# Performance work log

Hardware: AMD Instinct MI355X
Metric: run time of the kernel (lower is better)

## Reference

```python
import jax, jax.numpy as jnp
import numpy as np

E = 256   # embedding_channels
C = 128   # c
N1 = 512
N2 = 512
NE1 = 16384
NE2 = 16384
EPS = 1e-5


def _ln(x, w, b):
    m = x.mean(-1, keepdims=True)
    v = jnp.mean((x - m) ** 2, axis=-1, keepdims=True)
    return (x - m) * jax.lax.rsqrt(v + EPS) * w + b


def _lin(x, w, b):
    return x @ w.T + b


def setup_inputs() -> dict:
    key = jax.random.key(0)
    ks = jax.random.split(key, 12)
    p = lambda k, shape: jax.random.normal(k, shape, jnp.float32) * 0.02
    return {
        "z": jax.random.normal(ks[0], (N1, N2, E), jnp.float32),
        "efeat1": jax.random.normal(ks[1], (NE1, E), jnp.float32),
        "efeat2": jax.random.normal(ks[2], (NE2, E), jnp.float32),
        "ln_w": jnp.ones((E,), jnp.float32), "ln_b": jnp.zeros((E,), jnp.float32),
        "lnc_w": jnp.ones((C,), jnp.float32), "lnc_b": jnp.zeros((C,), jnp.float32),
        "gl1_w": p(ks[3], (C, E)), "gl1_b": jnp.zeros((C,), jnp.float32),
        "gl2_w": p(ks[4], (C, E)), "gl2_b": jnp.zeros((C,), jnp.float32),
        "l1_w": p(ks[5], (C, E)), "l1_b": jnp.zeros((C,), jnp.float32),
        "l2_w": p(ks[6], (C, E)), "l2_b": jnp.zeros((C,), jnp.float32),
        "eg_w": p(ks[7], (E, E)), "eg_b": jnp.zeros((E,), jnp.float32),
        "las_w": p(ks[8], (E, C)), "las_b": jnp.zeros((E,), jnp.float32),
        "edges1": jax.random.randint(ks[9], (2, NE1), 0, N1, jnp.int64 if jax.config.jax_enable_x64 else jnp.int32),
        "edges2": jax.random.randint(ks[10], (2, NE2), 0, N2, jnp.int64 if jax.config.jax_enable_x64 else jnp.int32),
    }


def reference(z, efeat1, efeat2, ln_w, ln_b, lnc_w, lnc_b, gl1_w, gl1_b,
              gl2_w, gl2_b, l1_w, l1_b, l2_w, l2_b, eg_w, eg_b,
              las_w, las_b, edges1, edges2):
    zl = _ln(z, ln_w, ln_b)                       # [n1,n2,E]
    p1 = _ln(efeat1, ln_w, ln_b)                  # [ne1,E]
    p2 = _ln(efeat2, ln_w, ln_b)                  # [ne2,E]

    gate = lambda x, gw, gb, lw, lb: jax.nn.sigmoid(_lin(x, gw, gb)) * _lin(x, lw, lb)
    ab1 = gate(zl, gl1_w, gl1_b, l1_w, l1_b)      # [n1,n2,C]
    ab2 = gate(zl, gl2_w, gl2_b, l2_w, l2_b)      # [n1,n2,C]
    p1 = gate(p1, gl1_w, gl1_b, l1_w, l1_b)       # [ne1,C]
    p2 = gate(p2, gl2_w, gl2_b, l2_w, l2_b)       # [ne2,C]
    g = jax.nn.sigmoid(_lin(zl, eg_w, eg_b))      # [n1,n2,E]

    n1, n2 = z.shape[0], z.shape[1]
    # sparse COO -> dense (duplicate indices sum, matching torch coalesce)
    P1 = jnp.zeros((n1, n1, C), z.dtype).at[edges1[0], edges1[1]].add(p1)
    P2 = jnp.zeros((n2, n2, C), z.dtype).at[edges2[0], edges2[1]].add(p2)

    block1 = jnp.einsum('ikc,kjc->ijc', P1, ab1)  # [n1,n2,C]
    block2 = jnp.einsum('ikc,jkc->ijc', ab2, P2)  # [n1,n2,C]

    return g * _lin(_ln(block1 + block2, lnc_w, lnc_b), las_w, las_b)
```

## Files before the change

kernel.cpp:

```cpp
#include <hip/hip_runtime.h>
#include <stdint.h>

#define NN 512
#define EE 256
#define CC 128
#define NEDGE 16384
#define RR (NN*NN)
#define RT3 (RR + 2*NEDGE)

using bf16x8 = __attribute__((ext_vector_type(8))) short;
using f32x4  = __attribute__((ext_vector_type(4))) float;

__device__ __forceinline__ unsigned short f2bf(float f) {
  union { float f; unsigned u; } v; v.f = f;
  unsigned r = v.u + 0x7FFFu + ((v.u >> 16) & 1u);
  return (unsigned short)(r >> 16);
}
__device__ __forceinline__ float bf2f(unsigned short h) {
  union { unsigned u; float f; } v; v.u = ((unsigned)h) << 16;
  return v.f;
}
__device__ __forceinline__ float sigm(float x) { return 1.f / (1.f + __expf(-x)); }

__global__ __launch_bounds__(256) void k_ln(
    const float* __restrict__ z, const float* __restrict__ e1,
    const float* __restrict__ e2, const float* __restrict__ lnw,
    const float* __restrict__ lnb, unsigned short* __restrict__ zl) {
  int row = blockIdx.x * 4 + (threadIdx.x >> 6);
  int lane = threadIdx.x & 63;
  const float* src;
  if (row < RR)            src = z  + (size_t)row * EE;
  else if (row < RR+NEDGE) src = e1 + (size_t)(row - RR) * EE;
  else                     src = e2 + (size_t)(row - RR - NEDGE) * EE;
  float4 v = ((const float4*)src)[lane];
  float s = v.x + v.y + v.z + v.w;
  float q = v.x*v.x + v.y*v.y + v.z*v.z + v.w*v.w;
  #pragma unroll
  for (int o = 32; o > 0; o >>= 1) { s += __shfl_xor(s, o); q += __shfl_xor(q, o); }
  float m = s * (1.f/EE);
  float rstd = rsqrtf(q*(1.f/EE) - m*m + 1e-5f);
  float4 wv = ((const float4*)lnw)[lane];
  float4 bv = ((const float4*)lnb)[lane];
  ushort4 o4;
  o4.x = f2bf((v.x - m)*rstd*wv.x + bv.x);
  o4.y = f2bf((v.y - m)*rstd*wv.y + bv.y);
  o4.z = f2bf((v.z - m)*rstd*wv.z + bv.z);
  o4.w = f2bf((v.w - m)*rstd*wv.w + bv.w);
  ((ushort4*)(zl + (size_t)row * EE))[lane] = o4;
}

__global__ __launch_bounds__(256) void k_wconv(
    const float* __restrict__ gl1, const float* __restrict__ l1,
    const float* __restrict__ gl2, const float* __restrict__ l2,
    const float* __restrict__ eg,  const float* __restrict__ las,
    unsigned short* __restrict__ Wcol, unsigned short* __restrict__ Wrow,
    unsigned short* __restrict__ Wlas) {
  int t = blockIdx.x * 256 + threadIdx.x;
  if (t < 65536) {
    Wcol[t] = f2bf(t < 32768 ? gl1[t] : l1[t - 32768]);
  } else if (t < 196608) {
    int u = t - 65536;
    float v = (u < 32768) ? gl2[u] : (u < 65536) ? l2[u - 32768] : eg[u - 65536];
    Wrow[u] = f2bf(v);
  } else {
    int u = t - 196608;
    Wlas[u] = f2bf(las[u]);
  }
}

__global__ __launch_bounds__(256) void k_proj_gate(
    const unsigned short* __restrict__ zl, const unsigned short* __restrict__ W,
    const float* __restrict__ gb, const float* __restrict__ lb,
    unsigned short* __restrict__ abOut, float* __restrict__ Pf,
    const int* __restrict__ edges, int mode) {
  __shared__ __attribute__((aligned(16))) short As[128*32];
  __shared__ __attribute__((aligned(16))) short Bg[128*32];
  __shared__ __attribute__((aligned(16))) short Bl[128*32];
  const int t = threadIdx.x, w = t >> 6, lane = t & 63;
  const int mt = blockIdx.x;
  const bool isE = (mt >= RR/128);
  size_t abase; int astride;
  if (!isE) {
    if (mode == 0) { int rt0 = mt*128; abase = (size_t)(rt0 & 511)*512 + (rt0 >> 9); astride = 512; }
    else           { abase = (size_t)mt*128; astride = 1; }
  } else {
    abase = (size_t)RR + (mode ? NEDGE : 0) + (mt*128 - RR); astride = 1;
  }
  const f32x4 z4 = {0.f, 0.f, 0.f, 0.f};
  f32x4 ag[4][4], al[4][4];
  #pragma unroll
  for (int a = 0; a < 4; ++a)
    #pragma unroll
    for (int b = 0; b < 4; ++b) { ag[a][b] = z4; al[a][b] = z4; }
  const int wr = (w >> 1)*64, wc = (w & 1)*64;
  #pragma unroll 1
  for (int kk = 0; kk < 8; ++kk) {
    const int k0 = kk * 32;
    __syncthreads();
    #pragma unroll
    for (int s2 = 0; s2 < 2; ++s2) {
      int sidx = t + s2*256, row = sidx >> 2, seg = sidx & 3;
      int lo = row*32 + seg*8;
      *(uint4*)&As[lo] = *(const uint4*)(zl + (abase + (size_t)row*astride)*EE + k0 + seg*8);
      const unsigned short* wp = W + (size_t)row*EE + k0 + seg*8;
      *(uint4*)&Bg[lo] = *(const uint4*)wp;
      *(uint4*)&Bl[lo] = *(const uint4*)(wp + 128*EE);
    }
    __syncthreads();
    bf16x8 af[4], bgf[4], blf[4];
    #pragma unroll
    for (int f = 0; f < 4; ++f) {
      af[f]  = *(const bf16x8*)&As[(wr + f*16 + (lane & 15))*32 + (lane >> 4)*8];
      bgf[f] = *(const bf16x8*)&Bg[(wc + f*16 + (lane & 15))*32 + (lane >> 4)*8];
      blf[f] = *(const bf16x8*)&Bl[(wc + f*16 + (lane & 15))*32 + (lane >> 4)*8];
    }
    #pragma unroll
    for (int fm = 0; fm < 4; ++fm)
      #pragma unroll
      for (int fn = 0; fn < 4; ++fn) {
        ag[fm][fn] = __builtin_amdgcn_mfma_f32_16x16x32_bf16(af[fm], bgf[fn], ag[fm][fn], 0, 0, 0);
        al[fm][fn] = __builtin_amdgcn_mfma_f32_16x16x32_bf16(af[fm], blf[fn], al[fm][fn], 0, 0, 0);
      }
  }
  const int quad = lane >> 4, lc = lane & 15;
  #pragma unroll
  for (int fm = 0; fm < 4; ++fm)
    #pragma unroll
    for (int fn = 0; fn < 4; ++fn) {
      int c = wc + fn*16 + lc;
      float bgv = gb[c], blv = lb[c];
      float v0 = sigm(ag[fm][fn][0] + bgv) * (al[fm][fn][0] + blv);
      float v1 = sigm(ag[fm][fn][1] + bgv) * (al[fm][fn][1] + blv);
      float v2 = sigm(ag[fm][fn][2] + bgv) * (al[fm][fn][2] + blv);
      float v3 = sigm(ag[fm][fn][3] + bgv) * (al[fm][fn][3] + blv);
      int rl = wr + fm*16 + quad*4;
      if (!isE) {
        size_t rt = (size_t)mt*128 + rl;
        ushort4 o; o.x = f2bf(v0); o.y = f2bf(v1); o.z = f2bf(v2); o.w = f2bf(v3);
        *(ushort4*)&abOut[(size_t)c*RR + rt] = o;
      } else {
        int e0 = mt*128 - RR + rl;
        float vv[4] = {v0, v1, v2, v3};
        #pragma unroll
        for (int rg = 0; rg < 4; ++rg) {
          int e = e0 + rg;
          int i0 = edges[e], i1 = edges[NEDGE + e];
          atomicAdd(&Pf[((size_t)i0*NN + i1)*CC + c], vv[rg]);
        }
      }
    }
}

__global__ __launch_bounds__(256) void k_proj_g(
    const unsigned short* __restrict__ zl, const unsigned short* __restrict__ Weg,
    const float* __restrict__ egb, unsigned short* __restrict__ gOut) {
  __shared__ __attribute__((aligned(16))) short As[128*32];
  __shared__ __attribute__((aligned(16))) short Bs[128*32];
  const int t = threadIdx.x, w = t >> 6, lane = t & 63;
  const int mt = blockIdx.x, half = blockIdx.y;
  const size_t abase = (size_t)mt * 128;
  const unsigned short* Wb = Weg + (size_t)half * 128 * EE;
  const f32x4 z4 = {0.f, 0.f, 0.f, 0.f};
  f32x4 acc[4][4];
  #pragma unroll
  for (int a = 0; a < 4; ++a)
    #pragma unroll
    for (int b = 0; b < 4; ++b) acc[a][b] = z4;
  const int wr = (w >> 1)*64, wc = (w & 1)*64;
  #pragma unroll 1
  for (int kk = 0; kk < 8; ++kk) {
    const int k0 = kk * 32;
    __syncthreads();
    #pragma unroll
    for (int s2 = 0; s2 < 2; ++s2) {
      int sidx = t + s2*256, row = sidx >> 2, seg = sidx & 3;
      int lo = row*32 + seg*8;
      *(uint4*)&As[lo] = *(const uint4*)(zl + (abase + row)*EE + k0 + seg*8);
      *(uint4*)&Bs[lo] = *(const uint4*)(Wb + (size_t)row*EE + k0 + seg*8);
    }
    __syncthreads();
    bf16x8 af[4], bf_[4];
    #pragma unroll
    for (int f = 0; f < 4; ++f) {
      af[f]  = *(const bf16x8*)&As[(wr + f*16 + (lane & 15))*32 + (lane >> 4)*8];
      bf_[f] = *(const bf16x8*)&Bs[(wc + f*16 + (lane & 15))*32 + (lane >> 4)*8];
    }
    #pragma unroll
    for (int fn = 0; fn < 4; ++fn)
      #pragma unroll
      for (int fm = 0; fm < 4; ++fm)
        acc[fn][fm] = __builtin_amdgcn_mfma_f32_16x16x32_bf16(bf_[fn], af[fm], acc[fn][fm], 0, 0, 0);
  }
  const int quad = lane >> 4, lc = lane & 15;
  #pragma unroll
  for (int fn = 0; fn < 4; ++fn) {
    int e = half*128 + wc + fn*16 + quad*4;
    float4 bv = *(const float4*)(egb + e);
    #pragma unroll
    for (int fm = 0; fm < 4; ++fm) {
      size_t r = (size_t)mt*128 + wr + fm*16 + lc;
      ushort4 o;
      o.x = f2bf(sigm(acc[fn][fm][0] + bv.x));
      o.y = f2bf(sigm(acc[fn][fm][1] + bv.y));
      o.z = f2bf(sigm(acc[fn][fm][2] + bv.z));
      o.w = f2bf(sigm(acc[fn][fm][3] + bv.w));
      *(ushort4*)&gOut[r*EE + e] = o;
    }
  }
}

__global__ __launch_bounds__(256) void k_pcvt(
    const float* __restrict__ P1f, const float* __restrict__ P2f,
    unsigned short* __restrict__ P1c, unsigned short* __restrict__ P2c) {
  const float* src = blockIdx.y ? P2f : P1f;
  unsigned short* dst = blockIdx.y ? P2c : P1c;
  __shared__ float Ls[128*65];
  const int t = threadIdx.x;
  const size_t pos0 = (size_t)blockIdx.x * 64;
  #pragma unroll
  for (int it = 0; it < 8; ++it) {
    int fi = t + it*256;
    int p = fi >> 5, cq = fi & 31;
    float4 v = ((const float4*)(src + (pos0 + p)*CC))[cq];
    Ls[(cq*4+0)*65 + p] = v.x; Ls[(cq*4+1)*65 + p] = v.y;
    Ls[(cq*4+2)*65 + p] = v.z; Ls[(cq*4+3)*65 + p] = v.w;
  }
  __syncthreads();
  #pragma unroll
  for (int it = 0; it < 8; ++it) {
    int oi = t + it*256;
    int c = oi >> 4, pq = oi & 15;
    ushort4 o;
    o.x = f2bf(Ls[c*65 + pq*4 + 0]); o.y = f2bf(Ls[c*65 + pq*4 + 1]);
    o.z = f2bf(Ls[c*65 + pq*4 + 2]); o.w = f2bf(Ls[c*65 + pq*4 + 3]);
    *(ushort4*)&dst[(size_t)c*RR + pos0 + pq*4] = o;
  }
}

__global__ __launch_bounds__(256) void k_einsum(
    const unsigned short* __restrict__ P1c, const unsigned short* __restrict__ ab1t,
    const unsigned short* __restrict__ ab2c, const unsigned short* __restrict__ P2c,
    float* __restrict__ Sf) {
  __shared__ __attribute__((aligned(16))) short A1s[128*32];
  __shared__ __attribute__((aligned(16))) short B1s[128*32];
  __shared__ __attribute__((aligned(16))) short A2s[128*32];
  __shared__ __attribute__((aligned(16))) short B2s[128*32];
  const int t = threadIdx.x, w = t >> 6, lane = t & 63;
  const int n = blockIdx.x;
  const int xcd = n & 7, bi = n >> 3;
  const int ch = xcd * 16 + (bi >> 4);
  const int tile = bi & 15;
  const int mt = tile & 3, nt = tile >> 2;
  const size_t cb = (size_t)ch * RR;
  const unsigned short* A1g = P1c  + cb + (size_t)mt*128*512;
  const unsigned short* B1g = ab1t + cb + (size_t)nt*128*512;
  const unsigned short* A2g = ab2c + cb + (size_t)mt*128*512;
  const unsigned short* B2g = P2c  + cb + (size_t)nt*128*512;
  const f32x4 z4 = {0.f, 0.f, 0.f, 0.f};
  f32x4 acc[4][4];
  #pragma unroll
  for (int a = 0; a < 4; ++a)
    #pragma unroll
    for (int b = 0; b < 4; ++b) acc[a][b] = z4;
  const int wr = (w >> 1)*64, wc = (w & 1)*64;
  #pragma unroll 1
  for (int kk = 0; kk < 16; ++kk) {
    const int k0 = kk * 32;
    __syncthreads();
    #pragma unroll
    for (int s2 = 0; s2 < 2; ++s2) {
      int sidx = t + s2*256, row = sidx >> 2, seg = sidx & 3;
      int go = row*512 + k0 + seg*8;
      int lo = row*32 + seg*8;
      *(uint4*)&A1s[lo] = *(const uint4*)(A1g + go);
      *(uint4*)&B1s[lo] = *(const uint4*)(B1g + go);
      *(uint4*)&A2s[lo] = *(const uint4*)(A2g + go);
      *(uint4*)&B2s[lo] = *(const uint4*)(B2g + go);
    }
    __syncthreads();
    bf16x8 a1[4], b1[4], a2[4], b2[4];
    #pragma unroll
    for (int f = 0; f < 4; ++f) {
      int ro = (wr + f*16 + (lane & 15))*32 + (lane >> 4)*8;
      int co = (wc + f*16 + (lane & 15))*32 + (lane >> 4)*8;
      a1[f] = *(const bf16x8*)&A1s[ro];
      a2[f] = *(const bf16x8*)&A2s[ro];
      b1[f] = *(const bf16x8*)&B1s[co];
      b2[f] = *(const bf16x8*)&B2s[co];
    }
    #pragma unroll
    for (int fm = 0; fm < 4; ++fm)
      #pragma unroll
      for (int fn = 0; fn < 4; ++fn) {
        acc[fm][fn] = __builtin_amdgcn_mfma_f32_16x16x32_bf16(a1[fm], b1[fn], acc[fm][fn], 0, 0, 0);
        acc[fm][fn] = __builtin_amdgcn_mfma_f32_16x16x32_bf16(a2[fm], b2[fn], acc[fm][fn], 0, 0, 0);
      }
  }
  const int quad = lane >> 4, lc = lane & 15;
  #pragma unroll
  for (int fm = 0; fm < 4; ++fm)
    #pragma unroll
    for (int fn = 0; fn < 4; ++fn) {
      int j = nt*128 + wc + fn*16 + lc;
      int ib = mt*128 + wr + fm*16 + quad*4;
      #pragma unroll
      for (int rg = 0; rg < 4; ++rg)
        Sf[cb + (size_t)(ib + rg)*NN + j] = acc[fm][fn][rg];
    }
}

__global__ __launch_bounds__(256) void k_out(
    const float* __restrict__ Sf, const unsigned short* __restrict__ g,
    const unsigned short* __restrict__ Wlas, const float* __restrict__ lasb,
    const float* __restrict__ lncw, const float* __restrict__ lncb,
    float* __restrict__ out) {
  __shared__ __attribute__((aligned(16))) char Als[64*256];
  const int t = threadIdx.x, w = t >> 6, lane = t & 63;
  const size_t r0 = (size_t)blockIdx.x * 64;
  const int row = t >> 2, part = t & 3;

  float x[32];
  const float* sp = Sf + (size_t)(part*32)*RR + r0 + row;
  #pragma unroll
  for (int i = 0; i < 32; ++i) x[i] = sp[(size_t)i*RR];
  float s = 0.f, q = 0.f;
  #pragma unroll
  for (int i = 0; i < 32; ++i) { s += x[i]; q += x[i]*x[i]; }
  s += __shfl_xor(s, 1); q += __shfl_xor(q, 1);
  s += __shfl_xor(s, 2); q += __shfl_xor(q, 2);
  float m = s * (1.f/CC);
  float rstd = rsqrtf(q*(1.f/CC) - m*m + 1e-5f);

  {
    const float4* wv4 = (const float4*)(lncw + part*32);
    const float4* bv4 = (const float4*)(lncb + part*32);
    #pragma unroll
    for (int i4 = 0; i4 < 8; ++i4) {
      float4 wv = wv4[i4], bv = bv4[i4];
      ushort4 o;
      o.x = f2bf((x[i4*4+0]-m)*rstd*wv.x + bv.x);
      o.y = f2bf((x[i4*4+1]-m)*rstd*wv.y + bv.y);
      o.z = f2bf((x[i4*4+2]-m)*rstd*wv.z + bv.z);
      o.w = f2bf((x[i4*4+3]-m)*rstd*wv.w + bv.w);
      int boff = (part*64 + i4*8) ^ ((row & 7) << 4);
      *(ushort4*)(Als + row*256 + boff) = o;
    }
  }
  __syncthreads();

  const int quad = lane >> 4, lc = lane & 15;
  const f32x4 z4 = {0.f, 0.f, 0.f, 0.f};
  f32x4 acc[4][4];
  #pragma unroll
  for (int a = 0; a < 4; ++a)
    #pragma unroll
    for (int b = 0; b < 4; ++b) acc[a][b] = z4;
  #pragma unroll
  for (int kk = 0; kk < 4; ++kk) {
    bf16x8 wf[4], sfr[4];
    #pragma unroll
    for (int f = 0; f < 4; ++f) {
      wf[f]  = *(const bf16x8*)(Wlas + (size_t)(w*64 + f*16 + lc)*CC + kk*32 + quad*8);
      int r = f*16 + lc;
      sfr[f] = *(const bf16x8*)(Als + r*256 + ((kk*64 + quad*16) ^ ((r & 7) << 4)));
    }
    #pragma unroll
    for (int fe = 0; fe < 4; ++fe)
      #pragma unroll
      for (int fr = 0; fr < 4; ++fr)
        acc[fe][fr] = __builtin_amdgcn_mfma_f32_16x16x32_bf16(wf[fe], sfr[fr], acc[fe][fr], 0, 0, 0);
  }

  #pragma unroll
  for (int fe = 0; fe < 4; ++fe) {
    const int e0 = w*64 + fe*16 + quad*4;
    const float4 lb = *(const float4*)(lasb + e0);
    #pragma unroll
    for (int fr = 0; fr < 4; ++fr) {
      const size_t r = r0 + fr*16 + lc;
      ushort4 gv = *(const ushort4*)(g + r*EE + e0);
      f32x4 v = acc[fe][fr];
      float4 o;
      o.x = bf2f(gv.x) * (v[0] + lb.x);
      o.y = bf2f(gv.y) * (v[1] + lb.y);
      o.z = bf2f(gv.z) * (v[2] + lb.z);
      o.w = bf2f(gv.w) * (v[3] + lb.w);
      *(float4*)&out[r*EE + e0] = o;
    }
  }
}

extern "C" void kernel_launch(void* const* d_in, const int* in_sizes, int n_in,
                              void* d_out, int out_size, void* d_ws, size_t ws_size,
                              hipStream_t stream) {
  const float* z    = (const float*)d_in[0];
  const float* ef1  = (const float*)d_in[1];
  const float* ef2  = (const float*)d_in[2];
  const float* lnw  = (const float*)d_in[3];
  const float* lnb  = (const float*)d_in[4];
  const float* lncw = (const float*)d_in[5];
  const float* lncb = (const float*)d_in[6];
  const float* gl1w = (const float*)d_in[7];
  const float* gl1b = (const float*)d_in[8];
  const float* gl2w = (const float*)d_in[9];
  const float* gl2b = (const float*)d_in[10];
  const float* l1w  = (const float*)d_in[11];
  const float* l1b  = (const float*)d_in[12];
  const float* l2w  = (const float*)d_in[13];
  const float* l2b  = (const float*)d_in[14];
  const float* egw  = (const float*)d_in[15];
  const float* egb  = (const float*)d_in[16];
  const float* lasw = (const float*)d_in[17];
  const float* lasb = (const float*)d_in[18];
  const int* edges1 = (const int*)d_in[19];
  const int* edges2 = (const int*)d_in[20];
  float* out = (float*)d_out;

  char* ws = (char*)d_ws;
  unsigned short* zl   = (unsigned short*)(ws);
  unsigned short* P1c  = (unsigned short*)(ws);
  unsigned short* P2c  = (unsigned short*)(ws + 67108864);
  unsigned short* ab1t = (unsigned short*)(ws + 150994944);
  unsigned short* ab2c = (unsigned short*)(ws + 218103808);
  unsigned short* gbuf = (unsigned short*)(ws + 285212672);
  float* P1f = (float*)(ws + 419430400);
  float* Sf  = (float*)(ws + 419430400);
  float* P2f = (float*)(ws + 553648128);
  unsigned short* Wcol = (unsigned short*)(ws + 687865856);
  unsigned short* Wrow = (unsigned short*)(ws + 687996928);
  unsigned short* Wlas = (unsigned short*)(ws + 688259072);

  hipMemsetAsync(P1f, 0, (size_t)RR*CC*4, stream);
  hipMemsetAsync(P2f, 0, (size_t)RR*CC*4, stream);
  k_wconv<<<896, 256, 0, stream>>>(gl1w, l1w, gl2w, l2w, egw, lasw, Wcol, Wrow, Wlas);
  k_ln<<<RT3/4, 256, 0, stream>>>(z, ef1, ef2, lnw, lnb, zl);
  k_proj_gate<<<2176, 256, 0, stream>>>(zl, Wcol, gl1b, l1b, ab1t, P1f, edges1, 0);
  k_proj_gate<<<2176, 256, 0, stream>>>(zl, Wrow, gl2b, l2b, ab2c, P2f, edges2, 1);
  k_proj_g<<<dim3(2048, 2), 256, 0, stream>>>(zl, Wrow + 256*EE, egb, gbuf);
  k_pcvt<<<dim3(4096, 2), 256, 0, stream>>>(P1f, P2f, P1c, P2c);
  k_einsum<<<2048, 256, 0, stream>>>(P1c, ab1t, ab2c, P2c, Sf);
  k_out<<<4096, 256, 0, stream>>>(Sf, gbuf, Wlas, lasb, lncw, lncb, out);
}
```

Baseline: 1.283 ms.

## Use async global-to-LDS loads, vectorize block stores, stage LN input via LDS

Replaces register-staged global-to-shared tile copies in the three GEMM kernels with global_load_lds direct-to-LDS transfers. The block einsum kernel swaps MFMA operand order so each lane holds four consecutive columns and can write float4 stores instead of scalar strided stores. The output kernel now loads its channel-major input tile with coalesced float4 reads into a padded LDS buffer and prefetches the gate values early to hide their latency. This adds LDS usage, which may lower occupancy, and depends on the async-load layout matching the previous shared memory layout.

```diff
diff --git a/kernel.cpp b/kernel.cpp
--- a/kernel.cpp
+++ b/kernel.cpp
@@ -21,6 +21,13 @@
   return v.f;
 }
 __device__ __forceinline__ float sigm(float x) { return 1.f / (1.f + __expf(-x)); }
+
+__device__ __forceinline__ void async16(const void* gp, void* lp) {
+  __builtin_amdgcn_global_load_lds(
+      (const __attribute__((address_space(1))) unsigned int*)(uintptr_t)gp,
+      (__attribute__((address_space(3))) unsigned int*)(unsigned)(uintptr_t)lp,
+      16, 0, 0);
+}
 
 __global__ __launch_bounds__(256) void k_ln(
     const float* __restrict__ z, const float* __restrict__ e1,
@@ -100,11 +107,11 @@
     #pragma unroll
     for (int s2 = 0; s2 < 2; ++s2) {
       int sidx = t + s2*256, row = sidx >> 2, seg = sidx & 3;
-      int lo = row*32 + seg*8;
-      *(uint4*)&As[lo] = *(const uint4*)(zl + (abase + (size_t)row*astride)*EE + k0 + seg*8);
+      const unsigned short* ap = zl + (abase + (size_t)row*astride)*EE + k0 + seg*8;
       const unsigned short* wp = W + (size_t)row*EE + k0 + seg*8;
-      *(uint4*)&Bg[lo] = *(const uint4*)wp;
-      *(uint4*)&Bl[lo] = *(const uint4*)(wp + 128*EE);
+      async16(ap, (char*)As + sidx*16);
+      async16(wp, (char*)Bg + sidx*16);
+      async16(wp + 128*EE, (char*)Bl + sidx*16);
     }
     __syncthreads();
     bf16x8 af[4], bgf[4], blf[4];
@@ -174,9 +181,8 @@
     #pragma unroll
     for (int s2 = 0; s2 < 2; ++s2) {
       int sidx = t + s2*256, row = sidx >> 2, seg = sidx & 3;
-      int lo = row*32 + seg*8;
-      *(uint4*)&As[lo] = *(const uint4*)(zl + (abase + row)*EE + k0 + seg*8);
-      *(uint4*)&Bs[lo] = *(const uint4*)(Wb + (size_t)row*EE + k0 + seg*8);
+      async16(zl + (abase + row)*EE + k0 + seg*8, (char*)As + sidx*16);
+      async16(Wb + (size_t)row*EE + k0 + seg*8,   (char*)Bs + sidx*16);
     }
     __syncthreads();
     bf16x8 af[4], bf_[4];
@@ -271,11 +277,12 @@
     for (int s2 = 0; s2 < 2; ++s2) {
       int sidx = t + s2*256, row = sidx >> 2, seg = sidx & 3;
       int go = row*512 + k0 + seg*8;
-      int lo = row*32 + seg*8;
-      *(uint4*)&A1s[lo] = *(const uint4*)(A1g + go);
-      *(uint4*)&B1s[lo] = *(const uint4*)(B1g + go);
-      *(uint4*)&A2s[lo] = *(const uint4*)(A2g + go);
-      *(uint4*)&B2s[lo] = *(const uint4*)(B2g + go);
+      char* lo = (char*)0 + sidx*16;
+      async16(A1g + go, (char*)A1s + sidx*16);
+      async16(B1g + go, (char*)B1s + sidx*16);
+      async16(A2g + go, (char*)A2s + sidx*16);
+      async16(B2g + go, (char*)B2s + sidx*16);
+      (void)lo;
     }
     __syncthreads();
     bf16x8 a1[4], b1[4], a2[4], b2[4];
@@ -289,23 +296,23 @@
       b2[f] = *(const bf16x8*)&B2s[co];
     }
     #pragma unroll
-    for (int fm = 0; fm < 4; ++fm)
+    for (int fn = 0; fn < 4; ++fn)
       #pragma unroll
-      for (int fn = 0; fn < 4; ++fn) {
-        acc[fm][fn] = __builtin_amdgcn_mfma_f32_16x16x32_bf16(a1[fm], b1[fn], acc[fm][fn], 0, 0, 0);
-        acc[fm][fn] = __builtin_amdgcn_mfma_f32_16x16x32_bf16(a2[fm], b2[fn], acc[fm][fn], 0, 0, 0);
+      for (int fm = 0; fm < 4; ++fm) {
+        acc[fn][fm] = __builtin_amdgcn_mfma_f32_16x16x32_bf16(b1[fn], a1[fm], acc[fn][fm], 0, 0, 0);
+        acc[fn][fm] = __builtin_amdgcn_mfma_f32_16x16x32_bf16(b2[fn], a2[fm], acc[fn][fm], 0, 0, 0);
       }
   }
   const int quad = lane >> 4, lc = lane & 15;
   #pragma unroll
-  for (int fm = 0; fm < 4; ++fm)
-    #pragma unroll
-    for (int fn = 0; fn < 4; ++fn) {
-      int j = nt*128 + wc + fn*16 + lc;
-      int ib = mt*128 + wr + fm*16 + quad*4;
-      #pragma unroll
-      for (int rg = 0; rg < 4; ++rg)
-        Sf[cb + (size_t)(ib + rg)*NN + j] = acc[fm][fn][rg];
+  for (int fn = 0; fn < 4; ++fn)
+    #pragma unroll
+    for (int fm = 0; fm < 4; ++fm) {
+      int jb = nt*128 + wc + fn*16 + quad*4;
+      int i  = mt*128 + wr + fm*16 + lc;
+      f32x4 v = acc[fn][fm];
+      float4 o; o.x = v[0]; o.y = v[1]; o.z = v[2]; o.w = v[3];
+      *(float4*)&Sf[cb + (size_t)i*NN + jb] = o;
     }
 }
 
@@ -314,15 +321,37 @@
     const unsigned short* __restrict__ Wlas, const float* __restrict__ lasb,
     const float* __restrict__ lncw, const float* __restrict__ lncb,
     float* __restrict__ out) {
+  __shared__ float Sls[64*129];
   __shared__ __attribute__((aligned(16))) char Als[64*256];
   const int t = threadIdx.x, w = t >> 6, lane = t & 63;
+  const int quad = lane >> 4, lc = lane & 15;
   const size_t r0 = (size_t)blockIdx.x * 64;
+
+  ushort4 gpre[4][4];
+  #pragma unroll
+  for (int fe = 0; fe < 4; ++fe) {
+    const int e0 = w*64 + fe*16 + quad*4;
+    #pragma unroll
+    for (int fr = 0; fr < 4; ++fr) {
+      const size_t r = r0 + fr*16 + lc;
+      gpre[fe][fr] = *(const ushort4*)(g + r*EE + e0);
+    }
+  }
+
+  #pragma unroll
+  for (int it = 0; it < 8; ++it) {
+    int fi = t + it*256;
+    int c = fi >> 4, rq = fi & 15;
+    float4 v = ((const float4*)(Sf + (size_t)c*RR + r0))[rq];
+    Sls[(rq*4+0)*129 + c] = v.x; Sls[(rq*4+1)*129 + c] = v.y;
+    Sls[(rq*4+2)*129 + c] = v.z; Sls[(rq*4+3)*129 + c] = v.w;
+  }
+  __syncthreads();
+
   const int row = t >> 2, part = t & 3;
-
   float x[32];
-  const float* sp = Sf + (size_t)(part*32)*RR + r0 + row;
-  #pragma unroll
-  for (int i = 0; i < 32; ++i) x[i] = sp[(size_t)i*RR];
+  #pragma unroll
+  for (int i = 0; i < 32; ++i) x[i] = Sls[row*129 + part*32 + i];
   float s = 0.f, q = 0.f;
   #pragma unroll
   for (int i = 0; i < 32; ++i) { s += x[i]; q += x[i]*x[i]; }
@@ -330,7 +359,6 @@
   s += __shfl_xor(s, 2); q += __shfl_xor(q, 2);
   float m = s * (1.f/CC);
   float rstd = rsqrtf(q*(1.f/CC) - m*m + 1e-5f);
-
   {
     const float4* wv4 = (const float4*)(lncw + part*32);
     const float4* bv4 = (const float4*)(lncb + part*32);
@@ -348,7 +376,6 @@
   }
   __syncthreads();
 
-  const int quad = lane >> 4, lc = lane & 15;
   const f32x4 z4 = {0.f, 0.f, 0.f, 0.f};
   f32x4 acc[4][4];
   #pragma unroll
@@ -378,7 +405,7 @@
     #pragma unroll
     for (int fr = 0; fr < 4; ++fr) {
       const size_t r = r0 + fr*16 + lc;
-      ushort4 gv = *(const ushort4*)(g + r*EE + e0);
+      ushort4 gv = gpre[fe][fr];
       f32x4 v = acc[fe][fr];
       float4 o;
       o.x = bf2f(gv.x) * (v[0] + lb.x);
```

New measurement: 1.271 ms. About the same (-1.0%).
